# Performance work log

Measured on AMD Instinct MI355X. Metric: run time of the kernel, lower is better.

Reference implementation:

```python
import jax, jax.numpy as jnp
import numpy as np

NP, NA, H, K, TAU = 4096, 2048, 128, 5, 1.0
NODE_N = {'paper': NP, 'author': NA}
RELS = [('pp', 'paper', 'paper'), ('aa', 'author', 'author'),
        ('pa', 'paper', 'author'), ('ap', 'author', 'paper')]


def setup_inputs():
    key = jax.random.key(0)
    ks = jax.random.split(key, 32)
    f32 = jnp.float32
    def nrm(k, shape, scale=1.0):
        return jax.random.normal(k, shape, f32) * scale
    Epp, Eaa, Epa, Eap = 131072, 65536, 131072, 131072
    inp = {
        'x_paper': nrm(ks[0], (NP, H)),
        'x_author': nrm(ks[1], (NA, H)),
        'ei_pp': jax.random.randint(ks[2], (2, Epp), 0, NP, dtype=jnp.int32),
        'ei_aa': jax.random.randint(ks[3], (2, Eaa), 0, NA, dtype=jnp.int32),
        'ei_pa': jnp.stack([jax.random.randint(ks[4], (Epa,), 0, NP, dtype=jnp.int32),
                            jax.random.randint(ks[5], (Epa,), 0, NA, dtype=jnp.int32)]),
        'ei_ap': jnp.stack([jax.random.randint(ks[6], (Eap,), 0, NA, dtype=jnp.int32),
                            jax.random.randint(ks[7], (Eap,), 0, NP, dtype=jnp.int32)]),
        'batch_paper': jnp.zeros((NP,), jnp.int32),
        'batch_author': jnp.zeros((NA,), jnp.int32),
        'index': 7,
    }
    s = H ** -0.5
    i = 8
    for t in ('paper', 'author'):
        for l in (0, 1):
            inp['Wself_%s%d' % (t, l)] = nrm(ks[i], (H, H), s); i += 1
    for r, _, _ in RELS:
        for l in (0, 1):
            inp['W%s%d' % (r, l)] = nrm(ks[i], (H, H), s); i += 1
    for r in ('pp', 'aa'):
        inp['Wep1_%s' % r] = nrm(ks[i], (2 * H, 256), (2 * H) ** -0.5); i += 1
        inp['bep1_%s' % r] = jnp.zeros((256,), f32)
        inp['Wep2_%s' % r] = nrm(ks[i], (256, 2), 256 ** -0.5); i += 1
        inp['bep2_%s' % r] = jnp.zeros((2,), f32)
    inp['Wc'] = nrm(ks[i], (H, 5), s)
    inp['bc'] = jnp.zeros((5,), f32)
    return inp


def _mean_agg(msg, dst, n):
    s = jax.ops.segment_sum(msg, dst, num_segments=n)
    c = jax.ops.segment_sum(jnp.ones((msg.shape[0], 1), msg.dtype), dst, num_segments=n)
    return s / jnp.maximum(c, 1.0)


def _gnn(x, ei, p, single, edge_attn=None):
    # 2-layer relation-typed mean-aggregation hetero GNN.
    h = dict(x)
    for l in (0, 1):
        nh = {}
        for t in ('paper', 'author'):
            agg = h[t] @ p['Wself_%s%d' % (t, l)]
            for r, s_t, d_t in RELS:
                if d_t != t or (single and s_t != d_t):
                    continue
                src, dst = ei[r][0], ei[r][1]
                msg = h[s_t][src] @ p['W%s%d' % (r, l)]  # [E, H]
                if edge_attn is not None and r in edge_attn:
                    msg = msg * edge_attn[r][:, None]
                agg = agg + _mean_agg(msg, dst, NODE_N[t])
            nh[t] = jax.nn.relu(agg)
        h = nh
    return h


def _edge_pred(h, ei, p, r, t):
    src, dst = ei[r][0], ei[r][1]
    e = jnp.concatenate([h[t][src], h[t][dst]], axis=-1)  # [E, 2H]
    e = jax.nn.relu(e @ p['Wep1_%s' % r] + p['bep1_%s' % r])
    return e @ p['Wep2_%s' % r] + p['bep2_%s' % r]  # [E, 2]


def _gumbel_topk(logits, mask, k, tau, key):
    # Masked straight-through top-k gumbel-softmax (row-wise, hard=True).
    u = jax.random.uniform(key, logits.shape, logits.dtype, 1e-10, 1.0)
    g = -jnp.log(-jnp.log(u))
    y = jnp.where(mask, (logits + g) / tau, -1e9)
    soft = jax.nn.softmax(y, axis=-1)
    _, idx = jax.lax.top_k(soft, k)  # [N, k]
    rows = jnp.arange(logits.shape[0])[:, None]
    hard = jnp.zeros_like(soft).at[rows, idx].set(1.0)
    return hard - jax.lax.stop_gradient(soft) + soft


def _prune(h, ei, p, r, t, n, key):
    pred = _edge_pred(h, ei, p, r, t)[:, 0]
    src, dst = ei[r][0], ei[r][1]
    # sparse_coo_tensor(...).to_dense(): duplicates coalesce by sum
    A = jnp.zeros((n, n), pred.dtype).at[src, dst].add(pred)
    S = _gumbel_topk(A, A > 0, K, TAU, key)
    return S[src, dst]


def _forward(p, ints):
    x = {'paper': p['x_paper'], 'author': p['x_author']}
    ei = {'pp': ints['ei_pp'], 'aa': ints['ei_aa'], 'pa': ints['ei_pa'], 'ap': ints['ei_ap']}
    h1 = _gnn(x, ei, p, single=True)
    kpp, kaa = jax.random.split(jax.random.key(42))
    w_pp = _prune(h1, ei, p, 'pp', 'paper', NP, kpp)
    w_aa = _prune(h1, ei, p, 'aa', 'author', NA, kaa)
    h2 = _gnn(x, ei, p, single=False, edge_attn={'pp': w_pp, 'aa': w_aa})
    pool = h2['paper'][ints['index']].reshape(1, -1)
    y_hat = pool @ p['Wc'] + p['bc']
    return y_hat, w_pp, w_aa


def reference(x_paper, x_author, ei_pp, ei_aa, ei_pa, ei_ap, batch_paper, batch_author, index,
              Wself_paper0, Wself_paper1, Wself_author0, Wself_author1,
              Wpp0, Wpp1, Waa0, Waa1, Wpa0, Wpa1, Wap0, Wap1,
              Wep1_pp, bep1_pp, Wep2_pp, bep2_pp, Wep1_aa, bep1_aa, Wep2_aa, bep2_aa,
              Wc, bc):
    p = dict(x_paper=x_paper, x_author=x_author,
             Wself_paper0=Wself_paper0, Wself_paper1=Wself_paper1,
             Wself_author0=Wself_author0, Wself_author1=Wself_author1,
             Wpp0=Wpp0, Wpp1=Wpp1, Waa0=Waa0, Waa1=Waa1,
             Wpa0=Wpa0, Wpa1=Wpa1, Wap0=Wap0, Wap1=Wap1,
             Wep1_pp=Wep1_pp, bep1_pp=bep1_pp, Wep2_pp=Wep2_pp, bep2_pp=bep2_pp,
             Wep1_aa=Wep1_aa, bep1_aa=bep1_aa, Wep2_aa=Wep2_aa, bep2_aa=bep2_aa,
             Wc=Wc, bc=bc)
    ints = dict(ei_pp=ei_pp, ei_aa=ei_aa, ei_pa=ei_pa, ei_ap=ei_ap, index=index)
    return _forward(p, ints)
```

## Files before the change

### kernel.cpp

```cpp
#include <hip/hip_runtime.h>
#include <stdint.h>


namespace {

constexpr int NPn = 4096;
constexpr int NAn = 2048;
constexpr int Hh  = 128;
constexpr int EPPc = 131072;
constexpr int EAAc = 65536;
constexpr int KSEL = 5;
constexpr int BSLOT = 128;


__host__ __device__ static inline void tf2x32(uint32_t k0, uint32_t k1,
                                              uint32_t& x0, uint32_t& x1) {
  uint32_t ks2 = k0 ^ k1 ^ 0x1BD11BDAu;
  x0 += k0; x1 += k1;
#define TF_R(r) { x0 += x1; x1 = (x1 << (r)) | (x1 >> (32 - (r))); x1 ^= x0; }
  TF_R(13) TF_R(15) TF_R(26) TF_R(6)
  x0 += k1;  x1 += ks2 + 1u;
  TF_R(17) TF_R(29) TF_R(16) TF_R(24)
  x0 += ks2; x1 += k0 + 2u;
  TF_R(13) TF_R(15) TF_R(26) TF_R(6)
  x0 += k0;  x1 += k1 + 3u;
  TF_R(17) TF_R(29) TF_R(16) TF_R(24)
  x0 += k1;  x1 += ks2 + 4u;
  TF_R(13) TF_R(15) TF_R(26) TF_R(6)
  x0 += ks2; x1 += k0 + 5u;
#undef TF_R
}

__global__ __launch_bounds__(256) void scatter_kernel(
    const int* src_pp, const int* dst_pp, const int* src_aa, const int* dst_aa,
    const int* src_pa, const int* dst_pa, const int* src_ap, const int* dst_ap,
    int* cnt, int* entries)
{
  int i = blockIdx.x * 256 + threadIdx.x;
  int key, pl;
  if (i < 131072) {
    int e = i;
    key = 0 + dst_pp[e]; pl = (src_pp[e] << 18) | e;
  } else if (i < 196608) {
    int e = i - 131072;
    key = 4096 + dst_aa[e]; pl = (src_aa[e] << 16) | e;
  } else if (i < 327680) {
    int e = i - 196608;
    key = 6144 + dst_pa[e]; pl = src_pa[e];
  } else if (i < 458752) {
    int e = i - 327680;
    key = 8192 + dst_ap[e]; pl = src_ap[e];
  } else if (i < 589824) {
    int e = i - 458752;
    key = 12288 + src_pp[e]; pl = (dst_pp[e] << 18) | e;
  } else if (i < 655360) {
    int e = i - 589824;
    key = 16384 + src_aa[e]; pl = (dst_aa[e] << 16) | e;
  } else return;
  int pos = atomicAdd(&cnt[key], 1);
  if (pos < BSLOT) entries[key * BSLOT + pos] = pl;
}

struct FDesc {
  const float* gsrc; const float* wArr; int cntOff; int shift;
  float* Mout;
  const float* Aself; const float* W0; const float* W1;
  const float* A2;  const float* W2;
  float* C; int relu;
  const float* WP; float* P1; float* P2;
};
struct FArgs { FDesc d[4]; int bstart[5]; int nd; };

__global__ __launch_bounds__(256) void fused_layer(FArgs fa, const int* __restrict__ cnt,
                                                   const int* __restrict__ entries)
{
  __shared__ __align__(16) float Ms[8][128];
  __shared__ __align__(16) float Xs[8][128];
  __shared__ __align__(16) float Zs[8][128];
  __shared__ __align__(16) float Ws[32][128];
  int blk = blockIdx.x, tid = threadIdx.x;
  int di = 0;
  while (di < fa.nd - 1 && blk >= fa.bstart[di + 1]) ++di;
  FDesc D = fa.d[di];
  int node0 = (blk - fa.bstart[di]) * 8;
  {
    int hw = tid >> 5;
    int node = node0 + hw;
    int fl = (tid & 31) << 2;
    int deg = cnt[D.cntOff + node];
    const int* ent = entries + (size_t)(D.cntOff + node) * BSLOT;
    const float* h = D.gsrc;
    int sh = D.shift;
    float ax = 0.f, ay = 0.f, az = 0.f, aw = 0.f;
    if (D.wArr) {
      unsigned mask = (1u << sh) - 1u;
      int k = 0;
      for (; k + 3 < deg; k += 4) {
        unsigned p0 = (unsigned)ent[k], p1 = (unsigned)ent[k + 1];
        unsigned p2 = (unsigned)ent[k + 2], p3 = (unsigned)ent[k + 3];
        float w0 = D.wArr[p0 & mask], w1 = D.wArr[p1 & mask];
        float w2v = D.wArr[p2 & mask], w3 = D.wArr[p3 & mask];
        float4 v0, v1, v2, v3;
        if (w0 != 0.f) v0 = *(const float4*)&h[(size_t)(p0 >> sh) * Hh + fl];
        if (w1 != 0.f) v1 = *(const float4*)&h[(size_t)(p1 >> sh) * Hh + fl];
        if (w2v != 0.f) v2 = *(const float4*)&h[(size_t)(p2 >> sh) * Hh + fl];
        if (w3 != 0.f) v3 = *(const float4*)&h[(size_t)(p3 >> sh) * Hh + fl];
        if (w0 != 0.f) { ax += v0.x; ay += v0.y; az += v0.z; aw += v0.w; }
        if (w1 != 0.f) { ax += v1.x; ay += v1.y; az += v1.z; aw += v1.w; }
        if (w2v != 0.f) { ax += v2.x; ay += v2.y; az += v2.z; aw += v2.w; }
        if (w3 != 0.f) { ax += v3.x; ay += v3.y; az += v3.z; aw += v3.w; }
      }
      for (; k < deg; ++k) {
        unsigned pl = (unsigned)ent[k];
        float wt = D.wArr[pl & mask];
        if (wt != 0.f) {
          float4 v = *(const float4*)&h[(size_t)(pl >> sh) * Hh + fl];
          ax += v.x; ay += v.y; az += v.z; aw += v.w;
        }
      }
    } else {
      int k = 0;
      for (; k + 7 < deg; k += 8) {
        unsigned p0 = (unsigned)ent[k],     p1 = (unsigned)ent[k + 1];
        unsigned p2 = (unsigned)ent[k + 2], p3 = (unsigned)ent[k + 3];
        unsigned p4 = (unsigned)ent[k + 4], p5 = (unsigned)ent[k + 5];
        unsigned p6 = (unsigned)ent[k + 6], p7 = (unsigned)ent[k + 7];
        float4 v0 = *(const float4*)&h[(size_t)(p0 >> sh) * Hh + fl];
        float4 v1 = *(const float4*)&h[(size_t)(p1 >> sh) * Hh + fl];
        float4 v2 = *(const float4*)&h[(size_t)(p2 >> sh) * Hh + fl];
        float4 v3 = *(const float4*)&h[(size_t)(p3 >> sh) * Hh + fl];
        float4 v4 = *(const float4*)&h[(size_t)(p4 >> sh) * Hh + fl];
        float4 v5 = *(const float4*)&h[(size_t)(p5 >> sh) * Hh + fl];
        float4 v6 = *(const float4*)&h[(size_t)(p6 >> sh) * Hh + fl];
        float4 v7 = *(const float4*)&h[(size_t)(p7 >> sh) * Hh + fl];
        ax += v0.x; ay += v0.y; az += v0.z; aw += v0.w;
        ax += v1.x; ay += v1.y; az += v1.z; aw += v1.w;
        ax += v2.x; ay += v2.y; az += v2.z; aw += v2.w;
        ax += v3.x; ay += v3.y; az += v3.z; aw += v3.w;
        ax += v4.x; ay += v4.y; az += v4.z; aw += v4.w;
        ax += v5.x; ay += v5.y; az += v5.z; aw += v5.w;
        ax += v6.x; ay += v6.y; az += v6.z; aw += v6.w;
        ax += v7.x; ay += v7.y; az += v7.z; aw += v7.w;
      }
      for (; k < deg; ++k) {
        unsigned pl = (unsigned)ent[k];
        float4 v = *(const float4*)&h[(size_t)(pl >> sh) * Hh + fl];
        ax += v.x; ay += v.y; az += v.z; aw += v.w;
      }
    }
    float cd = fmaxf((float)deg, 1.0f);
    float4 o; o.x = ax / cd; o.y = ay / cd; o.z = az / cd; o.w = aw / cd;
    if (D.W0 == nullptr) {
      *(float4*)&D.Mout[(size_t)node * Hh + fl] = o;
    } else {
      *(float4*)&Ms[hw][fl] = o;
    }
  }
  if (D.W0 == nullptr) return;
  {
    int rm = tid >> 5, cq = (tid & 31) << 2;
    *(float4*)&Xs[rm][cq] = *(const float4*)&D.Aself[(size_t)(node0 + rm) * 128 + cq];
    if (D.A2)
      *(float4*)&Zs[rm][cq] = *(const float4*)&D.A2[(size_t)(node0 + rm) * 128 + cq];
  }
  int m = tid >> 5, nq = tid & 31;
  float4 accv = {0.f, 0.f, 0.f, 0.f};
  int parts = D.A2 ? 3 : 2;
  for (int p = 0; p < parts; ++p) {
    const float* W = (p == 0) ? D.W0 : (p == 1) ? D.W1 : D.W2;
    for (int c = 0; c < 4; ++c) {
      __syncthreads();
      {
        int r = tid >> 3, f = (tid & 7) << 4;
        const float* srcp = &W[(size_t)(c * 32 + r) * 128 + f];
        *(float4*)&Ws[r][f]      = *(const float4*)&srcp[0];
        *(float4*)&Ws[r][f + 4]  = *(const float4*)&srcp[4];
        *(float4*)&Ws[r][f + 8]  = *(const float4*)&srcp[8];
        *(float4*)&Ws[r][f + 12] = *(const float4*)&srcp[12];
      }
      __syncthreads();
#define KCHUNK(AR)                                              \
      _Pragma("unroll")                                         \
      for (int k = 0; k < 32; ++k) {                            \
        float a = AR[m][c * 32 + k];                            \
        float4 wv = *(const float4*)&Ws[k][nq << 2];            \
        accv.x += a * wv.x; accv.y += a * wv.y;                 \
        accv.z += a * wv.z; accv.w += a * wv.w;                 \
      }
      if (p == 0) { KCHUNK(Xs) } else if (p == 1) { KCHUNK(Ms) } else { KCHUNK(Zs) }
#undef KCHUNK
    }
  }
  if (D.relu) {
    accv.x = fmaxf(accv.x, 0.f); accv.y = fmaxf(accv.y, 0.f);
    accv.z = fmaxf(accv.z, 0.f); accv.w = fmaxf(accv.w, 0.f);
  }
  if (D.C)
    *(float4*)&D.C[(size_t)(node0 + m) * 128 + (nq << 2)] = accv;
  if (D.WP == nullptr) return;
  __syncthreads();
  *(float4*)&Xs[m][nq << 2] = accv;
  __syncthreads();
  int c0 = nq << 3;
  float4 p1a = {0,0,0,0}, p1b = {0,0,0,0}, p2a = {0,0,0,0}, p2b = {0,0,0,0};
  for (int k = 0; k < 128; ++k) {
    float a = Xs[m][k];
    const float* w1 = &D.WP[(size_t)k * 256 + c0];
    const float* w2 = &D.WP[(size_t)(128 + k) * 256 + c0];
    float4 u1a = *(const float4*)&w1[0], u1b = *(const float4*)&w1[4];
    float4 u2a = *(const float4*)&w2[0], u2b = *(const float4*)&w2[4];
    p1a.x += a * u1a.x; p1a.y += a * u1a.y; p1a.z += a * u1a.z; p1a.w += a * u1a.w;
    p1b.x += a * u1b.x; p1b.y += a * u1b.y; p1b.z += a * u1b.z; p1b.w += a * u1b.w;
    p2a.x += a * u2a.x; p2a.y += a * u2a.y; p2a.z += a * u2a.z; p2a.w += a * u2a.w;
    p2b.x += a * u2b.x; p2b.y += a * u2b.y; p2b.z += a * u2b.z; p2b.w += a * u2b.w;
  }
  *(float4*)&D.P1[(size_t)(node0 + m) * 256 + c0]     = p1a;
  *(float4*)&D.P1[(size_t)(node0 + m) * 256 + c0 + 4] = p1b;
  *(float4*)&D.P2[(size_t)(node0 + m) * 256 + c0]     = p2a;
  *(float4*)&D.P2[(size_t)(node0 + m) * 256 + c0 + 4] = p2b;
}

__global__ __launch_bounds__(256) void row_topk(
    const float* __restrict__ P1pp, const float* __restrict__ P2pp,
    const float* __restrict__ b1pp, const float* __restrict__ W2pp,
    const float* __restrict__ b2pp,
    const float* __restrict__ P1aa, const float* __restrict__ P2aa,
    const float* __restrict__ b1aa, const float* __restrict__ W2aa,
    const float* __restrict__ b2aa,
    const int* __restrict__ cnt, const int* __restrict__ entries,
    float* __restrict__ w_pp, float* __restrict__ w_aa,
    uint32_t kpp0, uint32_t kpp1, uint32_t kaa0, uint32_t kaa1)
{
  __shared__ float P1s[256], b1s[256], w2s[256];
  __shared__ int   dS[128];
  __shared__ float pS[128];
  __shared__ int   sel5[KSEL];
  int blk = blockIdx.x, tid = threadIdx.x;
  int lane = tid & 63, wv = tid >> 6;
  int row, Ncols, shift, co; unsigned mask;
  const float* P1; const float* P2; const float* b1; const float* W2; const float* b2;
  float* wout; uint32_t k0, k1;
  if (blk < NPn) {
    row = blk; Ncols = NPn; shift = 18; mask = 0x3FFFFu; co = 12288;
    P1 = P1pp; P2 = P2pp; b1 = b1pp; W2 = W2pp; b2 = b2pp;
    wout = w_pp; k0 = kpp0; k1 = kpp1;
  } else {
    row = blk - NPn; Ncols = NAn; shift = 16; mask = 0xFFFFu; co = 16384;
    P1 = P1aa; P2 = P2aa; b1 = b1aa; W2 = W2aa; b2 = b2aa;
    wout = w_aa; k0 = kaa0; k1 = kaa1;
  }
  const int* ent = entries + (size_t)(co + row) * BSLOT;
  int deg = cnt[co + row];
  P1s[tid] = P1[(size_t)row * 256 + tid];
  b1s[tid] = b1[tid];
  w2s[tid] = W2[tid * 2];
  __syncthreads();
  float bias2 = b2[0];
  int j = lane << 2;
  for (int k = wv * 4; k < deg; k += 16) {
    int n = deg - k; if (n > 4) n = 4;
    unsigned pl0 = (unsigned)ent[k];
    unsigned pl1 = (n > 1) ? (unsigned)ent[k + 1] : pl0;
    unsigned pl2 = (n > 2) ? (unsigned)ent[k + 2] : pl0;
    unsigned pl3 = (n > 3) ? (unsigned)ent[k + 3] : pl0;
    int d0 = (int)(pl0 >> shift), d1 = (int)(pl1 >> shift);
    int d2 = (int)(pl2 >> shift), d3 = (int)(pl3 >> shift);
    float4 q0 = *(const float4*)&P2[(size_t)d0 * 256 + j];
    float4 q1 = *(const float4*)&P2[(size_t)d1 * 256 + j];
    float4 q2 = *(const float4*)&P2[(size_t)d2 * 256 + j];
    float4 q3 = *(const float4*)&P2[(size_t)d3 * 256 + j];
    float pa = P1s[j + 0], pb = P1s[j + 1], pc = P1s[j + 2], pd = P1s[j + 3];
    float ba = b1s[j + 0], bb = b1s[j + 1], bc_ = b1s[j + 2], bd = b1s[j + 3];
    float wa = w2s[j + 0], wb = w2s[j + 1], wc = w2s[j + 2], wd = w2s[j + 3];
    float s0 = fmaxf(pa + q0.x + ba, 0.f) * wa + fmaxf(pb + q0.y + bb, 0.f) * wb +
               fmaxf(pc + q0.z + bc_, 0.f) * wc + fmaxf(pd + q0.w + bd, 0.f) * wd;
    float s1 = fmaxf(pa + q1.x + ba, 0.f) * wa + fmaxf(pb + q1.y + bb, 0.f) * wb +
               fmaxf(pc + q1.z + bc_, 0.f) * wc + fmaxf(pd + q1.w + bd, 0.f) * wd;
    float s2 = fmaxf(pa + q2.x + ba, 0.f) * wa + fmaxf(pb + q2.y + bb, 0.f) * wb +
               fmaxf(pc + q2.z + bc_, 0.f) * wc + fmaxf(pd + q2.w + bd, 0.f) * wd;
    float s3 = fmaxf(pa + q3.x + ba, 0.f) * wa + fmaxf(pb + q3.y + bb, 0.f) * wb +
               fmaxf(pc + q3.z + bc_, 0.f) * wc + fmaxf(pd + q3.w + bd, 0.f) * wd;
    for (int off = 32; off; off >>= 1) {
      s0 += __shfl_down(s0, off);
      s1 += __shfl_down(s1, off);
      s2 += __shfl_down(s2, off);
      s3 += __shfl_down(s3, off);
    }
    if (lane == 0) {
      dS[k] = d0; pS[k] = s0 + bias2;
      if (n > 1) { dS[k + 1] = d1; pS[k + 1] = s1 + bias2; }
      if (n > 2) { dS[k + 2] = d2; pS[k + 2] = s2 + bias2; }
      if (n > 3) { dS[k + 3] = d3; pS[k + 3] = s3 + bias2; }
    }
  }
  __syncthreads();
  if (deg > 0 && wv == 0) {
    int   e0 = (lane < deg) ? dS[lane] : -1;
    float q0v = (lane < deg) ? pS[lane] : 0.f;
    bool  two = (deg > 64);
    int   e1 = -1; float q1v = 0.f;
    if (two && 64 + lane < deg) { e1 = dS[64 + lane]; q1v = pS[64 + lane]; }
    float a0 = 0.f, a1 = 0.f;
    bool lead0 = (e0 >= 0), lead1 = (e1 >= 0);
    for (int j2 = 0; j2 < deg; ++j2) {
      int bj; float bp;
      if (j2 < 64) { bj = __shfl(e0, j2); bp = __shfl(q0v, j2); }
      else         { bj = __shfl(e1, j2 - 64); bp = __shfl(q1v, j2 - 64); }
      if (e0 >= 0 && bj == e0) { a0 += bp; if (j2 < lane) lead0 = false; }
      if (e1 >= 0 && bj == e1) { a1 += bp; if (j2 < 64 + lane) lead1 = false; }
    }
    uint32_t rowbase = (uint32_t)row * (uint32_t)Ncols;
    float y0 = -1e9f, y1 = -1e9f;
    bool c0 = lead0 && (a0 > 0.f);
    if (c0) {
      uint32_t x0 = 0u, x1 = rowbase + (uint32_t)e0;
      tf2x32(k0, k1, x0, x1);
      uint32_t bits = x0 ^ x1;
      float fv = __uint_as_float((bits >> 9) | 0x3f800000u) - 1.0f;
      float u = fmaxf(1e-10f, fv + 1e-10f);
      y0 = a0 + (-logf(-logf(u)));
    }
    bool c1 = lead1 && (a1 > 0.f);
    if (c1) {
      uint32_t x0 = 0u, x1 = rowbase + (uint32_t)e1;
      tf2x32(k0, k1, x0, x1);
      uint32_t bits = x0 ^ x1;
      float fv = __uint_as_float((bits >> 9) | 0x3f800000u) - 1.0f;
      float u = fmaxf(1e-10f, fv + 1e-10f);
      y1 = a1 + (-logf(-logf(u)));
    }
    int cnt2 = __popcll(__ballot(c0)) + __popcll(__ballot(c1));
    int nsel = cnt2 < KSEL ? cnt2 : KSEL;
    for (int it = 0; it < nsel; ++it) {
      float best; int bc;
      if (y1 > y0 || (y1 == y0 && (unsigned)e1 < (unsigned)e0)) { best = y1; bc = e1; }
      else { best = y0; bc = e0; }
      for (int mm = 32; mm; mm >>= 1) {
        float ov = __shfl_xor(best, mm); int oc = __shfl_xor(bc, mm);
        if (ov > best || (ov == best && (unsigned)oc < (unsigned)bc)) { best = ov; bc = oc; }
      }
      if (lane == 0) sel5[it] = bc;
      if (e0 == bc) y0 = -3.0e38f;
      if (e1 == bc) y1 = -3.0e38f;
    }
    if (nsel < KSEL && lane == 0) {
      int c = 0;
      for (int it = nsel; it < KSEL; ++it) {
        for (;;) {
          bool used = false;
          for (int q = 0; q < it; ++q) used |= (sel5[q] == c);
          if (!used) break;
          ++c;
        }
        sel5[it] = c++;
      }
    }
  }
  __syncthreads();
  for (int k = tid; k < deg; k += 256) {
    unsigned pl = (unsigned)ent[k];
    int d = (int)(pl >> shift);
    int e = (int)(pl & mask);
    float v = 0.f;
#pragma unroll
    for (int q = 0; q < KSEL; ++q) v = (sel5[q] == d) ? 1.f : v;
    wout[e] = v;
  }
}

__global__ __launch_bounds__(128) void final_kernel(
    const float* __restrict__ hp, const float* __restrict__ ha,
    const int* __restrict__ idxPtr, const float* __restrict__ wpp,
    const int* __restrict__ cnt, const int* __restrict__ entries,
    const float* __restrict__ Wself, const float* __restrict__ Wpp,
    const float* __restrict__ Wap,
    const float* __restrict__ Wc, const float* __restrict__ bc,
    float* __restrict__ out)
{
  __shared__ float selfr[128], mpp[128], mapr[128], t[128];
  int tid = threadIdx.x;
  int idx = idxPtr[0];
  selfr[tid] = hp[(size_t)idx * 128 + tid];
  {
    int deg = cnt[idx];
    const int* ent = entries + (size_t)idx * BSLOT;
    float acc = 0.f;
    for (int k = 0; k < deg; ++k) {
      unsigned pl = (unsigned)ent[k];
      int s = (int)(pl >> 18);
      int e = (int)(pl & 0x3FFFFu);
      acc += wpp[e] * hp[(size_t)s * 128 + tid];
    }
    mpp[tid] = acc / fmaxf((float)deg, 1.0f);
  }
  {
    int deg = cnt[8192 + idx];
    const int* ent = entries + (size_t)(8192 + idx) * BSLOT;
    float acc = 0.f;
    for (int k = 0; k < deg; ++k) {
      int s = ent[k];
      acc += ha[(size_t)s * 128 + tid];
    }
    mapr[tid] = acc / fmaxf((float)deg, 1.0f);
  }
  __syncthreads();
  float s = 0.f;
  for (int m = 0; m < 128; ++m) {
    s += selfr[m] * Wself[m * 128 + tid] + mpp[m] * Wpp[m * 128 + tid] +
         mapr[m] * Wap[m * 128 + tid];
  }
  t[tid] = fmaxf(s, 0.f);
  __syncthreads();
  if (tid < 5) {
    float y = bc[tid];
    for (int k = 0; k < 128; ++k) y += t[k] * Wc[k * 5 + tid];
    out[tid] = y;
  }
}

}

extern "C" void kernel_launch(void* const* d_in, const int* in_sizes, int n_in,
                              void* d_out, int out_size, void* d_ws, size_t ws_size,
                              hipStream_t stream)
{
  (void)in_sizes; (void)n_in; (void)out_size; (void)ws_size;
  const float* x_p = (const float*)d_in[0];
  const float* x_a = (const float*)d_in[1];
  const int* ei_pp = (const int*)d_in[2];
  const int* ei_aa = (const int*)d_in[3];
  const int* ei_pa = (const int*)d_in[4];
  const int* ei_ap = (const int*)d_in[5];
  const int* idxPtr = (const int*)d_in[8];
  const float* Wself_p0 = (const float*)d_in[9];
  const float* Wself_p1 = (const float*)d_in[10];
  const float* Wself_a0 = (const float*)d_in[11];
  const float* Wself_a1 = (const float*)d_in[12];
  const float* Wpp0 = (const float*)d_in[13]; const float* Wpp1 = (const float*)d_in[14];
  const float* Waa0 = (const float*)d_in[15]; const float* Waa1 = (const float*)d_in[16];
  const float* Wpa0 = (const float*)d_in[17];
  const float* Wap0 = (const float*)d_in[19]; const float* Wap1 = (const float*)d_in[20];
  const float* Wep1_pp = (const float*)d_in[21]; const float* bep1_pp = (const float*)d_in[22];
  const float* Wep2_pp = (const float*)d_in[23]; const float* bep2_pp = (const float*)d_in[24];
  const float* Wep1_aa = (const float*)d_in[25]; const float* bep1_aa = (const float*)d_in[26];
  const float* Wep2_aa = (const float*)d_in[27]; const float* bep2_aa = (const float*)d_in[28];
  const float* Wc = (const float*)d_in[29]; const float* bc = (const float*)d_in[30];

  float* out = (float*)d_out;
  float* w_pp_out = out + 5;
  float* w_aa_out = out + 5 + EPPc;

  const int* src_pp = ei_pp;  const int* dst_pp = ei_pp + EPPc;
  const int* src_aa = ei_aa;  const int* dst_aa = ei_aa + EAAc;
  const int* src_pa = ei_pa;  const int* dst_pa = ei_pa + 131072;
  const int* src_ap = ei_ap;  const int* dst_ap = ei_ap + 131072;

  char* p = (char*)d_ws;
  auto alloc = [&](size_t bytes) -> void* {
    void* r = (void*)p;
    p += (bytes + 255) & ~(size_t)255;
    return r;
  };
  int* cnt     = (int*)alloc(18432 * sizeof(int));
  int* entries = (int*)alloc((size_t)18432 * BSLOT * sizeof(int));
  float* Map  = (float*)alloc((size_t)NPn * Hh * sizeof(float));
  float* Mpa  = (float*)alloc((size_t)NAn * Hh * sizeof(float));
  float* h1p0 = (float*)alloc((size_t)NPn * Hh * sizeof(float));
  float* h1a0 = (float*)alloc((size_t)NAn * Hh * sizeof(float));
  float* h2p0 = (float*)alloc((size_t)NPn * Hh * sizeof(float));
  float* h2a0 = (float*)alloc((size_t)NAn * Hh * sizeof(float));
  float* P1pp = (float*)alloc((size_t)NPn * 256 * sizeof(float));
  float* P2pp = (float*)alloc((size_t)NPn * 256 * sizeof(float));
  float* P1aa = (float*)alloc((size_t)NAn * 256 * sizeof(float));
  float* P2aa = (float*)alloc((size_t)NAn * 256 * sizeof(float));

  const int CO_PPD = 0, CO_AAD = 4096, CO_PAD = 6144, CO_APD = 8192;

  hipMemsetAsync(cnt, 0, 18432 * sizeof(int), stream);
  scatter_kernel<<<2560, 256, 0, stream>>>(src_pp, dst_pp, src_aa, dst_aa,
                                           src_pa, dst_pa, src_ap, dst_ap,
                                           cnt, entries);

  {
    FArgs fa{};
    fa.d[0] = {x_p, nullptr, CO_PPD, 18, nullptr,
               x_p, Wself_p0, Wpp0, nullptr, nullptr, h1p0, 1,
               nullptr, nullptr, nullptr};
    fa.d[1] = {x_a, nullptr, CO_AAD, 16, nullptr,
               x_a, Wself_a0, Waa0, nullptr, nullptr, h1a0, 1,
               nullptr, nullptr, nullptr};
    fa.d[2] = {x_a, nullptr, CO_APD, 0, Map,
               nullptr, nullptr, nullptr, nullptr, nullptr, nullptr, 0,
               nullptr, nullptr, nullptr};
    fa.d[3] = {x_p, nullptr, CO_PAD, 0, Mpa,
               nullptr, nullptr, nullptr, nullptr, nullptr, nullptr, 0,
               nullptr, nullptr, nullptr};
    fa.bstart[0] = 0; fa.bstart[1] = 512; fa.bstart[2] = 768;
    fa.bstart[3] = 1280; fa.bstart[4] = 1536; fa.nd = 4;
    fused_layer<<<1536, 256, 0, stream>>>(fa, cnt, entries);
  }

  {
    FArgs fa{};
    fa.d[0] = {h1p0, nullptr, CO_PPD, 18, nullptr,
               h1p0, Wself_p1, Wpp1, nullptr, nullptr, nullptr, 1,
               Wep1_pp, P1pp, P2pp};
    fa.d[1] = {h1a0, nullptr, CO_AAD, 16, nullptr,
               h1a0, Wself_a1, Waa1, nullptr, nullptr, nullptr, 1,
               Wep1_aa, P1aa, P2aa};
    fa.bstart[0] = 0; fa.bstart[1] = 512; fa.bstart[2] = 768; fa.nd = 2;
    fused_layer<<<768, 256, 0, stream>>>(fa, cnt, entries);
  }

  uint32_t kpp0, kpp1, kaa0, kaa1;
  { uint32_t a0 = 0, a1 = 0; tf2x32(0u, 42u, a0, a1); kpp0 = a0; kpp1 = a1; }
  { uint32_t a0 = 0, a1 = 1; tf2x32(0u, 42u, a0, a1); kaa0 = a0; kaa1 = a1; }

  row_topk<<<NPn + NAn, 256, 0, stream>>>(P1pp, P2pp, bep1_pp, Wep2_pp, bep2_pp,
                                          P1aa, P2aa, bep1_aa, Wep2_aa, bep2_aa,
                                          cnt, entries, w_pp_out, w_aa_out,
                                          kpp0, kpp1, kaa0, kaa1);

  {
    FArgs fa{};
    fa.d[0] = {x_p, w_pp_out, CO_PPD, 18, nullptr,
               x_p, Wself_p0, Wpp0, Map, Wap0, h2p0, 1,
               nullptr, nullptr, nullptr};
    fa.d[1] = {x_a, w_aa_out, CO_AAD, 16, nullptr,
               x_a, Wself_a0, Waa0, Mpa, Wpa0, h2a0, 1,
               nullptr, nullptr, nullptr};
    fa.bstart[0] = 0; fa.bstart[1] = 512; fa.bstart[2] = 768; fa.nd = 2;
    fused_layer<<<768, 256, 0, stream>>>(fa, cnt, entries);
  }

  final_kernel<<<1, 128, 0, stream>>>(h2p0, h2a0, idxPtr, w_pp_out,
                                      cnt, entries,
                                      Wself_p1, Wpp1, Wap1, Wc, bc, out);
}
```

Baseline: 359.7 us.

## Process 16 nodes per block and stage edge-predictor weights in shared memory

Each fused_layer block now handles 16 nodes instead of 8, so every weight tile loaded into shared memory serves twice as many rows, and each thread computes 8 output columns. The edge-predictor projection (WP) was read straight from global memory by every thread; it is now tiled through shared memory in 16-row chunks. Grid sizes are halved to match. The cost is fewer blocks per launch, which cuts parallelism for the gather phase on a large GPU, plus more registers per thread.

```diff
diff --git a/kernel.cpp b/kernel.cpp
--- a/kernel.cpp
+++ b/kernel.cpp
@@ -74,150 +74,172 @@
 __global__ __launch_bounds__(256) void fused_layer(FArgs fa, const int* __restrict__ cnt,
                                                    const int* __restrict__ entries)
 {
-  __shared__ __align__(16) float Ms[8][128];
-  __shared__ __align__(16) float Xs[8][128];
-  __shared__ __align__(16) float Zs[8][128];
-  __shared__ __align__(16) float Ws[32][128];
+  __shared__ __align__(16) float Ms[16 * 128];
+  __shared__ __align__(16) float Xs[16 * 128];
+  __shared__ __align__(16) float Zs[16 * 128];
+  __shared__ __align__(16) float Wst[4096];
   int blk = blockIdx.x, tid = threadIdx.x;
   int di = 0;
   while (di < fa.nd - 1 && blk >= fa.bstart[di + 1]) ++di;
   FDesc D = fa.d[di];
-  int node0 = (blk - fa.bstart[di]) * 8;
+  int node0 = (blk - fa.bstart[di]) * 16;
   {
     int hw = tid >> 5;
-    int node = node0 + hw;
     int fl = (tid & 31) << 2;
-    int deg = cnt[D.cntOff + node];
-    const int* ent = entries + (size_t)(D.cntOff + node) * BSLOT;
-    const float* h = D.gsrc;
-    int sh = D.shift;
-    float ax = 0.f, ay = 0.f, az = 0.f, aw = 0.f;
-    if (D.wArr) {
-      unsigned mask = (1u << sh) - 1u;
-      int k = 0;
-      for (; k + 3 < deg; k += 4) {
-        unsigned p0 = (unsigned)ent[k], p1 = (unsigned)ent[k + 1];
-        unsigned p2 = (unsigned)ent[k + 2], p3 = (unsigned)ent[k + 3];
-        float w0 = D.wArr[p0 & mask], w1 = D.wArr[p1 & mask];
-        float w2v = D.wArr[p2 & mask], w3 = D.wArr[p3 & mask];
-        float4 v0, v1, v2, v3;
-        if (w0 != 0.f) v0 = *(const float4*)&h[(size_t)(p0 >> sh) * Hh + fl];
-        if (w1 != 0.f) v1 = *(const float4*)&h[(size_t)(p1 >> sh) * Hh + fl];
-        if (w2v != 0.f) v2 = *(const float4*)&h[(size_t)(p2 >> sh) * Hh + fl];
-        if (w3 != 0.f) v3 = *(const float4*)&h[(size_t)(p3 >> sh) * Hh + fl];
-        if (w0 != 0.f) { ax += v0.x; ay += v0.y; az += v0.z; aw += v0.w; }
-        if (w1 != 0.f) { ax += v1.x; ay += v1.y; az += v1.z; aw += v1.w; }
-        if (w2v != 0.f) { ax += v2.x; ay += v2.y; az += v2.z; aw += v2.w; }
-        if (w3 != 0.f) { ax += v3.x; ay += v3.y; az += v3.z; aw += v3.w; }
-      }
-      for (; k < deg; ++k) {
-        unsigned pl = (unsigned)ent[k];
-        float wt = D.wArr[pl & mask];
-        if (wt != 0.f) {
+    for (int rep = 0; rep < 2; ++rep) {
+      int nloc = hw + rep * 8;
+      int node = node0 + nloc;
+      int deg = cnt[D.cntOff + node];
+      const int* ent = entries + (size_t)(D.cntOff + node) * BSLOT;
+      const float* h = D.gsrc;
+      int sh = D.shift;
+      float ax = 0.f, ay = 0.f, az = 0.f, aw = 0.f;
+      if (D.wArr) {
+        unsigned mask = (1u << sh) - 1u;
+        int k = 0;
+        for (; k + 3 < deg; k += 4) {
+          unsigned p0 = (unsigned)ent[k], p1 = (unsigned)ent[k + 1];
+          unsigned p2 = (unsigned)ent[k + 2], p3 = (unsigned)ent[k + 3];
+          float w0 = D.wArr[p0 & mask], w1 = D.wArr[p1 & mask];
+          float w2v = D.wArr[p2 & mask], w3 = D.wArr[p3 & mask];
+          float4 v0, v1, v2, v3;
+          if (w0 != 0.f) v0 = *(const float4*)&h[(size_t)(p0 >> sh) * Hh + fl];
+          if (w1 != 0.f) v1 = *(const float4*)&h[(size_t)(p1 >> sh) * Hh + fl];
+          if (w2v != 0.f) v2 = *(const float4*)&h[(size_t)(p2 >> sh) * Hh + fl];
+          if (w3 != 0.f) v3 = *(const float4*)&h[(size_t)(p3 >> sh) * Hh + fl];
+          if (w0 != 0.f) { ax += v0.x; ay += v0.y; az += v0.z; aw += v0.w; }
+          if (w1 != 0.f) { ax += v1.x; ay += v1.y; az += v1.z; aw += v1.w; }
+          if (w2v != 0.f) { ax += v2.x; ay += v2.y; az += v2.z; aw += v2.w; }
+          if (w3 != 0.f) { ax += v3.x; ay += v3.y; az += v3.z; aw += v3.w; }
+        }
+        for (; k < deg; ++k) {
+          unsigned pl = (unsigned)ent[k];
+          float wt = D.wArr[pl & mask];
+          if (wt != 0.f) {
+            float4 v = *(const float4*)&h[(size_t)(pl >> sh) * Hh + fl];
+            ax += v.x; ay += v.y; az += v.z; aw += v.w;
+          }
+        }
+      } else {
+        int k = 0;
+        for (; k + 7 < deg; k += 8) {
+          unsigned p0 = (unsigned)ent[k],     p1 = (unsigned)ent[k + 1];
+          unsigned p2 = (unsigned)ent[k + 2], p3 = (unsigned)ent[k + 3];
+          unsigned p4 = (unsigned)ent[k + 4], p5 = (unsigned)ent[k + 5];
+          unsigned p6 = (unsigned)ent[k + 6], p7 = (unsigned)ent[k + 7];
+          float4 v0 = *(const float4*)&h[(size_t)(p0 >> sh) * Hh + fl];
+          float4 v1 = *(const float4*)&h[(size_t)(p1 >> sh) * Hh + fl];
+          float4 v2 = *(const float4*)&h[(size_t)(p2 >> sh) * Hh + fl];
+          float4 v3 = *(const float4*)&h[(size_t)(p3 >> sh) * Hh + fl];
+          float4 v4 = *(const float4*)&h[(size_t)(p4 >> sh) * Hh + fl];
+          float4 v5 = *(const float4*)&h[(size_t)(p5 >> sh) * Hh + fl];
+          float4 v6 = *(const float4*)&h[(size_t)(p6 >> sh) * Hh + fl];
+          float4 v7 = *(const float4*)&h[(size_t)(p7 >> sh) * Hh + fl];
+          ax += v0.x; ay += v0.y; az += v0.z; aw += v0.w;
+          ax += v1.x; ay += v1.y; az += v1.z; aw += v1.w;
+          ax += v2.x; ay += v2.y; az += v2.z; aw += v2.w;
+          ax += v3.x; ay += v3.y; az += v3.z; aw += v3.w;
+          ax += v4.x; ay += v4.y; az += v4.z; aw += v4.w;
+          ax += v5.x; ay += v5.y; az += v5.z; aw += v5.w;
+          ax += v6.x; ay += v6.y; az += v6.z; aw += v6.w;
+          ax += v7.x; ay += v7.y; az += v7.z; aw += v7.w;
+        }
+        for (; k < deg; ++k) {
+          unsigned pl = (unsigned)ent[k];
           float4 v = *(const float4*)&h[(size_t)(pl >> sh) * Hh + fl];
           ax += v.x; ay += v.y; az += v.z; aw += v.w;
         }
       }
-    } else {
-      int k = 0;
-      for (; k + 7 < deg; k += 8) {
-        unsigned p0 = (unsigned)ent[k],     p1 = (unsigned)ent[k + 1];
-        unsigned p2 = (unsigned)ent[k + 2], p3 = (unsigned)ent[k + 3];
-        unsigned p4 = (unsigned)ent[k + 4], p5 = (unsigned)ent[k + 5];
-        unsigned p6 = (unsigned)ent[k + 6], p7 = (unsigned)ent[k + 7];
-        float4 v0 = *(const float4*)&h[(size_t)(p0 >> sh) * Hh + fl];
-        float4 v1 = *(const float4*)&h[(size_t)(p1 >> sh) * Hh + fl];
-        float4 v2 = *(const float4*)&h[(size_t)(p2 >> sh) * Hh + fl];
-        float4 v3 = *(const float4*)&h[(size_t)(p3 >> sh) * Hh + fl];
-        float4 v4 = *(const float4*)&h[(size_t)(p4 >> sh) * Hh + fl];
-        float4 v5 = *(const float4*)&h[(size_t)(p5 >> sh) * Hh + fl];
-        float4 v6 = *(const float4*)&h[(size_t)(p6 >> sh) * Hh + fl];
-        float4 v7 = *(const float4*)&h[(size_t)(p7 >> sh) * Hh + fl];
-        ax += v0.x; ay += v0.y; az += v0.z; aw += v0.w;
-        ax += v1.x; ay += v1.y; az += v1.z; aw += v1.w;
-        ax += v2.x; ay += v2.y; az += v2.z; aw += v2.w;
-        ax += v3.x; ay += v3.y; az += v3.z; aw += v3.w;
-        ax += v4.x; ay += v4.y; az += v4.z; aw += v4.w;
-        ax += v5.x; ay += v5.y; az += v5.z; aw += v5.w;
-        ax += v6.x; ay += v6.y; az += v6.z; aw += v6.w;
-        ax += v7.x; ay += v7.y; az += v7.z; aw += v7.w;
-      }
-      for (; k < deg; ++k) {
-        unsigned pl = (unsigned)ent[k];
-        float4 v = *(const float4*)&h[(size_t)(pl >> sh) * Hh + fl];
-        ax += v.x; ay += v.y; az += v.z; aw += v.w;
-      }
-    }
-    float cd = fmaxf((float)deg, 1.0f);
-    float4 o; o.x = ax / cd; o.y = ay / cd; o.z = az / cd; o.w = aw / cd;
-    if (D.W0 == nullptr) {
-      *(float4*)&D.Mout[(size_t)node * Hh + fl] = o;
-    } else {
-      *(float4*)&Ms[hw][fl] = o;
+      float cd = fmaxf((float)deg, 1.0f);
+      float4 o; o.x = ax / cd; o.y = ay / cd; o.z = az / cd; o.w = aw / cd;
+      if (D.W0 == nullptr) {
+        *(float4*)&D.Mout[(size_t)node * Hh + fl] = o;
+      } else {
+        *(float4*)&Ms[nloc * 128 + fl] = o;
+      }
     }
   }
   if (D.W0 == nullptr) return;
   {
-    int rm = tid >> 5, cq = (tid & 31) << 2;
-    *(float4*)&Xs[rm][cq] = *(const float4*)&D.Aself[(size_t)(node0 + rm) * 128 + cq];
-    if (D.A2)
-      *(float4*)&Zs[rm][cq] = *(const float4*)&D.A2[(size_t)(node0 + rm) * 128 + cq];
-  }
-  int m = tid >> 5, nq = tid & 31;
-  float4 accv = {0.f, 0.f, 0.f, 0.f};
+    int rm = tid >> 4;
+    int cq = (tid & 15) << 3;
+    *(float4*)&Xs[rm * 128 + cq]     = *(const float4*)&D.Aself[(size_t)(node0 + rm) * 128 + cq];
+    *(float4*)&Xs[rm * 128 + cq + 4] = *(const float4*)&D.Aself[(size_t)(node0 + rm) * 128 + cq + 4];
+    if (D.A2) {
+      *(float4*)&Zs[rm * 128 + cq]     = *(const float4*)&D.A2[(size_t)(node0 + rm) * 128 + cq];
+      *(float4*)&Zs[rm * 128 + cq + 4] = *(const float4*)&D.A2[(size_t)(node0 + rm) * 128 + cq + 4];
+    }
+  }
+  int m = tid >> 4, colq = tid & 15;
+  float4 acc0 = {0.f, 0.f, 0.f, 0.f}, acc1 = {0.f, 0.f, 0.f, 0.f};
   int parts = D.A2 ? 3 : 2;
   for (int p = 0; p < parts; ++p) {
     const float* W = (p == 0) ? D.W0 : (p == 1) ? D.W1 : D.W2;
+    const float* AR = (p == 0) ? Xs : (p == 1) ? Ms : Zs;
     for (int c = 0; c < 4; ++c) {
       __syncthreads();
-      {
-        int r = tid >> 3, f = (tid & 7) << 4;
-        const float* srcp = &W[(size_t)(c * 32 + r) * 128 + f];
-        *(float4*)&Ws[r][f]      = *(const float4*)&srcp[0];
-        *(float4*)&Ws[r][f + 4]  = *(const float4*)&srcp[4];
-        *(float4*)&Ws[r][f + 8]  = *(const float4*)&srcp[8];
-        *(float4*)&Ws[r][f + 12] = *(const float4*)&srcp[12];
+#pragma unroll
+      for (int jj = 0; jj < 4; ++jj) {
+        *(float4*)&Wst[jj * 1024 + tid * 4] =
+            *(const float4*)&W[(size_t)(c * 32 + jj * 8 + (tid >> 5)) * 128 + ((tid & 31) << 2)];
       }
       __syncthreads();
-#define KCHUNK(AR)                                              \
-      _Pragma("unroll")                                         \
-      for (int k = 0; k < 32; ++k) {                            \
-        float a = AR[m][c * 32 + k];                            \
-        float4 wv = *(const float4*)&Ws[k][nq << 2];            \
-        accv.x += a * wv.x; accv.y += a * wv.y;                 \
-        accv.z += a * wv.z; accv.w += a * wv.w;                 \
-      }
-      if (p == 0) { KCHUNK(Xs) } else if (p == 1) { KCHUNK(Ms) } else { KCHUNK(Zs) }
-#undef KCHUNK
+#pragma unroll
+      for (int k = 0; k < 32; ++k) {
+        float a = AR[m * 128 + c * 32 + k];
+        float4 w0 = *(const float4*)&Wst[k * 128 + colq * 8];
+        float4 w1 = *(const float4*)&Wst[k * 128 + colq * 8 + 4];
+        acc0.x += a * w0.x; acc0.y += a * w0.y; acc0.z += a * w0.z; acc0.w += a * w0.w;
+        acc1.x += a * w1.x; acc1.y += a * w1.y; acc1.z += a * w1.z; acc1.w += a * w1.w;
+      }
     }
   }
   if (D.relu) {
-    accv.x = fmaxf(accv.x, 0.f); accv.y = fmaxf(accv.y, 0.f);
-    accv.z = fmaxf(accv.z, 0.f); accv.w = fmaxf(accv.w, 0.f);
-  }
-  if (D.C)
-    *(float4*)&D.C[(size_t)(node0 + m) * 128 + (nq << 2)] = accv;
+    acc0.x = fmaxf(acc0.x, 0.f); acc0.y = fmaxf(acc0.y, 0.f);
+    acc0.z = fmaxf(acc0.z, 0.f); acc0.w = fmaxf(acc0.w, 0.f);
+    acc1.x = fmaxf(acc1.x, 0.f); acc1.y = fmaxf(acc1.y, 0.f);
+    acc1.z = fmaxf(acc1.z, 0.f); acc1.w = fmaxf(acc1.w, 0.f);
+  }
+  if (D.C) {
+    *(float4*)&D.C[(size_t)(node0 + m) * 128 + colq * 8]     = acc0;
+    *(float4*)&D.C[(size_t)(node0 + m) * 128 + colq * 8 + 4] = acc1;
+  }
   if (D.WP == nullptr) return;
   __syncthreads();
-  *(float4*)&Xs[m][nq << 2] = accv;
-  __syncthreads();
-  int c0 = nq << 3;
-  float4 p1a = {0,0,0,0}, p1b = {0,0,0,0}, p2a = {0,0,0,0}, p2b = {0,0,0,0};
-  for (int k = 0; k < 128; ++k) {
-    float a = Xs[m][k];
-    const float* w1 = &D.WP[(size_t)k * 256 + c0];
-    const float* w2 = &D.WP[(size_t)(128 + k) * 256 + c0];
-    float4 u1a = *(const float4*)&w1[0], u1b = *(const float4*)&w1[4];
-    float4 u2a = *(const float4*)&w2[0], u2b = *(const float4*)&w2[4];
-    p1a.x += a * u1a.x; p1a.y += a * u1a.y; p1a.z += a * u1a.z; p1a.w += a * u1a.w;
-    p1b.x += a * u1b.x; p1b.y += a * u1b.y; p1b.z += a * u1b.z; p1b.w += a * u1b.w;
-    p2a.x += a * u2a.x; p2a.y += a * u2a.y; p2a.z += a * u2a.z; p2a.w += a * u2a.w;
-    p2b.x += a * u2b.x; p2b.y += a * u2b.y; p2b.z += a * u2b.z; p2b.w += a * u2b.w;
-  }
-  *(float4*)&D.P1[(size_t)(node0 + m) * 256 + c0]     = p1a;
-  *(float4*)&D.P1[(size_t)(node0 + m) * 256 + c0 + 4] = p1b;
-  *(float4*)&D.P2[(size_t)(node0 + m) * 256 + c0]     = p2a;
-  *(float4*)&D.P2[(size_t)(node0 + m) * 256 + c0 + 4] = p2b;
+  *(float4*)&Xs[m * 128 + colq * 8]     = acc0;
+  *(float4*)&Xs[m * 128 + colq * 8 + 4] = acc1;
+  for (int half = 0; half < 2; ++half) {
+    float4 pA = {0,0,0,0}, pB = {0,0,0,0}, pC = {0,0,0,0}, pD = {0,0,0,0};
+    for (int kc = 0; kc < 8; ++kc) {
+      __syncthreads();
+#pragma unroll
+      for (int jj = 0; jj < 4; ++jj) {
+        *(float4*)&Wst[jj * 1024 + tid * 4] =
+            *(const float4*)&D.WP[(size_t)(half * 128 + kc * 16 + jj * 4 + (tid >> 6)) * 256 +
+                                  ((tid & 63) << 2)];
+      }
+      __syncthreads();
+#pragma unroll
+      for (int k = 0; k < 16; ++k) {
+        float a = Xs[m * 128 + kc * 16 + k];
+        int base = k * 256 + colq * 16;
+        float4 w0 = *(const float4*)&Wst[base];
+        float4 w1 = *(const float4*)&Wst[base + 4];
+        float4 w2 = *(const float4*)&Wst[base + 8];
+        float4 w3 = *(const float4*)&Wst[base + 12];
+        pA.x += a * w0.x; pA.y += a * w0.y; pA.z += a * w0.z; pA.w += a * w0.w;
+        pB.x += a * w1.x; pB.y += a * w1.y; pB.z += a * w1.z; pB.w += a * w1.w;
+        pC.x += a * w2.x; pC.y += a * w2.y; pC.z += a * w2.z; pC.w += a * w2.w;
+        pD.x += a * w3.x; pD.y += a * w3.y; pD.z += a * w3.z; pD.w += a * w3.w;
+      }
+    }
+    float* PD = half ? D.P2 : D.P1;
+    size_t ob = (size_t)(node0 + m) * 256 + colq * 16;
+    *(float4*)&PD[ob]      = pA;
+    *(float4*)&PD[ob + 4]  = pB;
+    *(float4*)&PD[ob + 8]  = pC;
+    *(float4*)&PD[ob + 12] = pD;
+  }
 }
 
 __global__ __launch_bounds__(256) void row_topk(
@@ -495,9 +517,9 @@
     fa.d[3] = {x_p, nullptr, CO_PAD, 0, Mpa,
                nullptr, nullptr, nullptr, nullptr, nullptr, nullptr, 0,
                nullptr, nullptr, nullptr};
-    fa.bstart[0] = 0; fa.bstart[1] = 512; fa.bstart[2] = 768;
-    fa.bstart[3] = 1280; fa.bstart[4] = 1536; fa.nd = 4;
-    fused_layer<<<1536, 256, 0, stream>>>(fa, cnt, entries);
+    fa.bstart[0] = 0; fa.bstart[1] = 256; fa.bstart[2] = 384;
+    fa.bstart[3] = 640; fa.bstart[4] = 768; fa.nd = 4;
+    fused_layer<<<768, 256, 0, stream>>>(fa, cnt, entries);
   }
 
   {
@@ -508,8 +530,8 @@
     fa.d[1] = {h1a0, nullptr, CO_AAD, 16, nullptr,
                h1a0, Wself_a1, Waa1, nullptr, nullptr, nullptr, 1,
                Wep1_aa, P1aa, P2aa};
-    fa.bstart[0] = 0; fa.bstart[1] = 512; fa.bstart[2] = 768; fa.nd = 2;
-    fused_layer<<<768, 256, 0, stream>>>(fa, cnt, entries);
+    fa.bstart[0] = 0; fa.bstart[1] = 256; fa.bstart[2] = 384; fa.nd = 2;
+    fused_layer<<<384, 256, 0, stream>>>(fa, cnt, entries);
   }
 
   uint32_t kpp0, kpp1, kaa0, kaa1;
@@ -529,8 +551,8 @@
     fa.d[1] = {x_a, w_aa_out, CO_AAD, 16, nullptr,
                x_a, Wself_a0, Waa0, Mpa, Wpa0, h2a0, 1,
                nullptr, nullptr, nullptr};
-    fa.bstart[0] = 0; fa.bstart[1] = 512; fa.bstart[2] = 768; fa.nd = 2;
-    fused_layer<<<768, 256, 0, stream>>>(fa, cnt, entries);
+    fa.bstart[0] = 0; fa.bstart[1] = 256; fa.bstart[2] = 384; fa.nd = 2;
+    fused_layer<<<384, 256, 0, stream>>>(fa, cnt, entries);
   }
 
   final_kernel<<<1, 128, 0, stream>>>(h2p0, h2a0, idxPtr, w_pp_out,
```

Result: slower. 431.6 us (+20.0%).
